# Kernel tuning notes

Hardware: AMD Instinct MI355X
Metric: run time of the kernel (lower is better)

The kernel has to match this reference:

```python
import jax, jax.numpy as jnp
import numpy as np

B, N = 1, 1024
VOCAB = 32000
DIM = 512
DEPTH = 2
HEADS = 8
DIM_HEAD = 64
DIM_INNER = HEADS * DIM_HEAD      # 512
DIM_FF = 4 * DIM                  # 2048
MAX_SEQ = 1024
EPS = 1e-12


def sq_dist(x, w):
    # squared L2 distance between rows of x [..., d] and rows of w [m, d] -> [..., m]
    xs = jnp.sum(x * x, axis=-1, keepdims=True)
    ws = jnp.sum(w * w, axis=-1)
    return xs - 2.0 * jnp.einsum('...d,md->...m', x, w) + ws


def cdist(x, w):
    # euclidean distance (torch.cdist equivalent)
    return jnp.sqrt(jnp.maximum(sq_dist(x, w), 0.0))


def rmsnorm(x, gamma):
    # F.normalize(x, dim=-1) * sqrt(dim) * (gamma + 1)
    n = jnp.linalg.norm(x, axis=-1, keepdims=True)
    return x / jnp.maximum(n, EPS) * (DIM ** 0.5) * (gamma + 1.0)


def attention(x, qkv_w, out_w):
    b, n, _ = x.shape
    qkv = cdist(x, qkv_w)                                   # [b, n, 3*inner] (to_qkv: squared=False)
    qkv = qkv.reshape(b, n, 3, HEADS, DIM_HEAD)
    qkv = qkv.transpose(2, 0, 3, 1, 4)                      # [3, b, h, n, d]
    q, k, v = qkv[0], qkv[1], qkv[2]
    qs = jnp.sum(q * q, axis=-1)                            # [b, h, n]
    ks = jnp.sum(k * k, axis=-1)                            # [b, h, n]
    # -||q_i - k_j||^2 = 2 q.k - ||q||^2 - ||k||^2
    sim = (2.0 * jnp.einsum('bhid,bhjd->bhij', q, k)
           - qs[..., :, None] - ks[..., None, :]) * (DIM_HEAD ** -0.5)
    attn = jax.nn.softmax(sim, axis=-1)
    o = jnp.einsum('bhij,bhjd->bhid', attn, v)
    o = o.transpose(0, 2, 1, 3).reshape(b, n, DIM_INNER)    # merge heads
    return o @ out_w.T                                      # plain Linear, no bias


def feedforward(x, w_in, b_in, w_out):
    h = -sq_dist(x, w_in) + b_in                            # proj_in: squared=True, negate=True, bias
    h = jax.nn.gelu(h, approximate=False)
    return h @ w_out.T                                      # plain Linear, no bias


def setup_inputs() -> dict:
    key = jax.random.key(0)
    ks = jax.random.split(key, 12)
    nrm = lambda k, s: jax.random.normal(k, s, dtype=jnp.float32)
    return {
        'tokens': jax.random.randint(ks[0], (B, N), 0, VOCAB),
        'token_emb': nrm(ks[1], (VOCAB, DIM)),
        'pos_emb': nrm(ks[2], (MAX_SEQ, DIM)),
        'qkv_w': nrm(ks[3], (DEPTH, 3 * DIM_INNER, DIM)),
        'attn_out_w': nrm(ks[4], (DEPTH, DIM, DIM_INNER)) * 0.02,
        'ff_in_w': nrm(ks[5], (DEPTH, DIM_FF, DIM)),
        'ff_in_b': nrm(ks[6], (DEPTH, DIM_FF)),
        'ff_out_w': nrm(ks[7], (DEPTH, DIM, DIM_FF)) * 0.02,
        'attn_gamma': jnp.zeros((DEPTH, DIM), jnp.float32),
        'ff_gamma': jnp.zeros((DEPTH, DIM), jnp.float32),
        'final_gamma': jnp.zeros((DIM,), jnp.float32),
    }


def reference(tokens, token_emb, pos_emb, qkv_w, attn_out_w, ff_in_w, ff_in_b,
              ff_out_w, attn_gamma, ff_gamma, final_gamma):
    n = tokens.shape[-1]
    x = token_emb[tokens] + pos_emb[:n]                     # [b, n, dim]
    for l in range(DEPTH):
        x = attention(rmsnorm(x, attn_gamma[l]), qkv_w[l], attn_out_w[l]) + x
        x = feedforward(rmsnorm(x, ff_gamma[l]), ff_in_w[l], ff_in_b[l], ff_out_w[l]) + x
    x = rmsnorm(x, final_gamma)
    return -sq_dist(x, token_emb)                           # [b, n, vocab] logits
```

## Files before the change

### kernel.cpp

```cpp
#include <hip/hip_runtime.h>
#include <math.h>

#define DIMM  512
#define NSEQ  1024
#define NHEAD 8
#define DH    64
#define DFF   2048
#define NVOC  32000
#define NDEPTH 2
#define VCENTER 32.0f
#define KVB   64
#define QBLK  32
#define QKOFF ((size_t)NHEAD * NSEQ * DH)
#define FLASH_BLOCKS (NSEQ / QBLK * NHEAD)
#define CONV_ROWS_PER_LAYER (NVOC / NDEPTH)
#define CONV_BLOCKS (CONV_ROWS_PER_LAYER / 64)

typedef __attribute__((ext_vector_type(8))) __bf16 bf16x8;
typedef __attribute__((ext_vector_type(4))) __bf16 bf16x4;
typedef __attribute__((ext_vector_type(4))) float f32x4;

__device__ __forceinline__ void g2l16(const void* g, void* l) {
    __builtin_amdgcn_global_load_lds(
        (const __attribute__((address_space(1))) void*)g,
        (__attribute__((address_space(3))) void*)l, 16, 0, 0);
}

#define WAITV(N) asm volatile("s_waitcnt vmcnt(" #N ")" ::: "memory")

__launch_bounds__(256)
__global__ void embed_rms(const int* __restrict__ tokens,
                          const float* __restrict__ temb,
                          const float* __restrict__ pemb,
                          const float* __restrict__ gamma,
                          float* __restrict__ x,
                          __bf16* __restrict__ y, float* __restrict__ xs) {
    int i = blockIdx.x;
    int tid = threadIdx.x;
    int tok = tokens[i];
    const float* e = temb + (size_t)tok * DIMM;
    const float* p = pemb + (size_t)i * DIMM;
    float v0 = e[tid] + p[tid];
    float v1 = e[tid + 256] + p[tid + 256];
    x[(size_t)i * DIMM + tid]       = v0;
    x[(size_t)i * DIMM + tid + 256] = v1;
    float ss = v0 * v0 + v1 * v1;
    __shared__ float red[4];
    #pragma unroll
    for (int off = 32; off; off >>= 1) ss += __shfl_down(ss, off, 64);
    if ((tid & 63) == 0) red[tid >> 6] = ss;
    __syncthreads();
    float tot = red[0] + red[1] + red[2] + red[3];
    float scale = 22.627416997969522f / fmaxf(sqrtf(tot), 1e-12f);
    float y0 = v0 * scale * (gamma[tid] + 1.0f);
    float y1 = v1 * scale * (gamma[tid + 256] + 1.0f);
    y[(size_t)i * DIMM + tid]       = (__bf16)y0;
    y[(size_t)i * DIMM + tid + 256] = (__bf16)y1;
    float s2 = y0 * y0 + y1 * y1;
    __syncthreads();
    #pragma unroll
    for (int off = 32; off; off >>= 1) s2 += __shfl_down(s2, off, 64);
    if ((tid & 63) == 0) red[tid >> 6] = s2;
    __syncthreads();
    if (tid == 0) xs[i] = red[0] + red[1] + red[2] + red[3];
}

template<int S>
__launch_bounds__(256)
__global__ void rms_red(const float* __restrict__ parts, float* __restrict__ x,
                        const float* __restrict__ gamma,
                        __bf16* __restrict__ y, float* __restrict__ xs) {
    int i = blockIdx.x;
    int tid = threadIdx.x;
    float* xr = x + (size_t)i * DIMM;
    float v0 = xr[tid], v1 = xr[tid + 256];
    #pragma unroll
    for (int s = 0; s < S; s++) {
        const float* pr = parts + (size_t)s * NSEQ * DIMM + (size_t)i * DIMM;
        v0 += pr[tid];
        v1 += pr[tid + 256];
    }
    xr[tid] = v0;
    xr[tid + 256] = v1;
    float ss = v0 * v0 + v1 * v1;
    __shared__ float red[4];
    #pragma unroll
    for (int off = 32; off; off >>= 1) ss += __shfl_down(ss, off, 64);
    if ((tid & 63) == 0) red[tid >> 6] = ss;
    __syncthreads();
    float tot = red[0] + red[1] + red[2] + red[3];
    float scale = 22.627416997969522f / fmaxf(sqrtf(tot), 1e-12f);
    float y0 = v0 * scale * (gamma[tid] + 1.0f);
    float y1 = v1 * scale * (gamma[tid + 256] + 1.0f);
    y[(size_t)i * DIMM + tid]       = (__bf16)y0;
    y[(size_t)i * DIMM + tid + 256] = (__bf16)y1;
    float s2 = y0 * y0 + y1 * y1;
    __syncthreads();
    #pragma unroll
    for (int off = 32; off; off >>= 1) s2 += __shfl_down(s2, off, 64);
    if ((tid & 63) == 0) red[tid >> 6] = s2;
    __syncthreads();
    if (tid == 0) xs[i] = red[0] + red[1] + red[2] + red[3];
}

__launch_bounds__(256)
__global__ void conv_all(const float* __restrict__ qkv_w, const float* __restrict__ attn_out_w,
                         const float* __restrict__ ff_in_w, const float* __restrict__ ff_out_w,
                         __bf16* __restrict__ wq16, __bf16* __restrict__ wa16,
                         __bf16* __restrict__ wfi16, __bf16* __restrict__ wfo16,
                         float* __restrict__ wsq_qkv, float* __restrict__ wsq_ff) {
    int bid = blockIdx.x;
    const float* src; __bf16* dst; float* ssq; int K = DIMM;
    if (bid < NDEPTH * 3 * DIMM) {
        src = qkv_w;  dst = wq16;  ssq = wsq_qkv;
    } else if ((bid -= NDEPTH * 3 * DIMM) < NDEPTH * DIMM) {
        src = attn_out_w; dst = wa16; ssq = nullptr;
    } else if ((bid -= NDEPTH * DIMM) < NDEPTH * DFF) {
        src = ff_in_w; dst = wfi16; ssq = wsq_ff;
    } else {
        bid -= NDEPTH * DFF;
        src = ff_out_w; dst = wfo16; ssq = nullptr; K = DFF;
    }
    const float* s = src + (size_t)bid * K;
    __bf16* d = dst + (size_t)bid * K;
    float ss = 0.f;
    for (int j = threadIdx.x; j < K; j += 256) {
        float v = s[j];
        d[j] = (__bf16)v;
        ss += v * v;
    }
    __shared__ float red[4];
    #pragma unroll
    for (int off = 32; off; off >>= 1) ss += __shfl_down(ss, off, 64);
    if ((threadIdx.x & 63) == 0) red[threadIdx.x >> 6] = ss;
    __syncthreads();
    if (threadIdx.x == 0 && ssq) ssq[bid] = red[0] + red[1] + red[2] + red[3];
}

enum { MODE_LINEAR = 0, MODE_CDIST = 1, MODE_FFGELU = 2, MODE_LOGITS = 3 };

template<int MODE>
__device__ __forceinline__ void write_elem(void* Cout, int r, int c, int M, float dot,
                                           float xsr, const float* __restrict__ ws,
                                           const float* __restrict__ bias) {
    if (MODE == MODE_LINEAR) {
        ((float*)Cout)[(size_t)r * M + c] = dot;
    } else if (MODE == MODE_FFGELU) {
        float d2 = xsr + ws[c] - 2.0f * dot;
        float hh = -d2 + bias[c];
        float v = 0.5f * hh * (1.0f + erff(hh * 0.70710678118654752f));
        ((__bf16*)Cout)[(size_t)r * M + c] = (__bf16)v;
    }
}

__launch_bounds__(512)
__global__ void gemm_logits(const __bf16* __restrict__ A, const __bf16* __restrict__ W,
                            const float* __restrict__ xs, const float* __restrict__ ws,
                            float* __restrict__ out) {
    __shared__ __align__(16) __bf16 As[6 * 128 * 32];
    __shared__ __align__(16) __bf16 Bs[6 * 256 * 32];
    const int tid = threadIdx.x;
    const int lane = tid & 63;
    const int wv = tid >> 6;
    const int wr = wv >> 2, wc = wv & 3;

    int id = blockIdx.x;
    id = (id & 7) * 125 + (id >> 3);
    const int row0 = (id & 7) * 128;
    const int col0 = (id >> 3) * 256;

    const int scol = ((tid & 3) ^ ((tid >> 3) & 3)) * 8;
    const __bf16* gA = A + (size_t)(row0 + (tid >> 2)) * DIMM + scol;
    const __bf16* gB = W + (size_t)(col0 + (tid >> 2)) * DIMM + scol;
    const int lrow = lane & 15;
    const int l4 = lane >> 4;
    const int slot = (l4 ^ ((lrow >> 1) & 3)) * 8;

    auto stageChunk = [&](int k0, int b) {
        g2l16(gA + k0,                      &As[b * 4096 + tid * 8]);
        g2l16(gB + k0,                      &Bs[b * 8192 + tid * 8]);
        g2l16(gB + (size_t)128 * DIMM + k0, &Bs[b * 8192 + 4096 + tid * 8]);
    };

    f32x4 acc[4][4] = {};
    const int nP = DIMM >> 6;
    stageChunk(0, 0);  stageChunk(32, 1);
    stageChunk(64, 2); stageChunk(96, 3);
    int pb = 0;
    for (int p = 0; p < nP; p++) {
        if (p < nP - 1) WAITV(6); else WAITV(0);
        __builtin_amdgcn_s_barrier();
        __builtin_amdgcn_sched_barrier(0);
        if (p + 2 < nP) {
            int nb = pb + 2; if (nb >= 3) nb -= 3;
            stageChunk((p + 2) << 6,        nb * 2);
            stageChunk(((p + 2) << 6) + 32, nb * 2 + 1);
        }
        #pragma unroll
        for (int half = 0; half < 2; half++) {
            const int b = pb * 2 + half;
            bf16x8 af[4], bfr[4];
            #pragma unroll
            for (int m = 0; m < 4; m++)
                af[m] = *(const bf16x8*)&As[b * 4096 + (wr * 64 + m * 16 + lrow) * 32 + slot];
            #pragma unroll
            for (int n = 0; n < 4; n++)
                bfr[n] = *(const bf16x8*)&Bs[b * 8192 + (wc * 64 + n * 16 + lrow) * 32 + slot];
            #pragma unroll
            for (int m = 0; m < 4; m++)
                #pragma unroll
                for (int n = 0; n < 4; n++)
                    acc[m][n] = __builtin_amdgcn_mfma_f32_16x16x32_bf16(af[m], bfr[n], acc[m][n], 0, 0, 0);
        }
        if (++pb == 3) pb = 0;
    }

    const int r_base = row0 + wr * 64 + l4 * 4;
    const int c_base = col0 + wc * 64 + lrow;
    #pragma unroll
    for (int m = 0; m < 4; m++)
        #pragma unroll
        for (int j = 0; j < 4; j++) {
            const int r = r_base + m * 16 + j;
            const float xsr = xs[r];
            #pragma unroll
            for (int n = 0; n < 4; n++) {
                const int c = c_base + n * 16;
                out[(size_t)r * NVOC + c] = -(xsr + ws[c] - 2.0f * acc[m][n][j]);
            }
        }
}

template<int MODE>
__launch_bounds__(256)
__global__ void gemm64(const __bf16* __restrict__ A, const __bf16* __restrict__ W,
                       const float* __restrict__ xs, const float* __restrict__ ws,
                       const float* __restrict__ bias,
                       void* __restrict__ Cout, int K, int Kstr, int M,
                       float* __restrict__ ksout) {
    __shared__ __align__(16) __bf16 As[6 * 64 * 32];
    __shared__ __align__(16) __bf16 Bs[6 * 64 * 32];
    __shared__ float ksred[2][64];
    const int tid = threadIdx.x;
    const int lane = tid & 63;
    const int wv = tid >> 6;
    const int wr = wv >> 1, wc = wv & 1;

    const int gx = gridDim.x;
    const int total = gx * gridDim.y;
    int id = blockIdx.y * gx + blockIdx.x;
    id = (id & 7) * (total >> 3) + (id >> 3);
    const int bx = id % gx;
    const int by = id / gx;
    const int row0 = by * 64;
    const int col0 = bx * 64;
    const size_t zoff = (size_t)blockIdx.z * K;
    float* Cz = (float*)Cout + (size_t)blockIdx.z * NSEQ * M;

    const int scol = (((tid & 3) ^ ((tid >> 3) & 3))) * 8;
    const __bf16* gA = A + (size_t)(row0 + (tid >> 2)) * Kstr + scol + zoff;
    const __bf16* gB = W + (size_t)(col0 + (tid >> 2)) * Kstr + scol + zoff;
    const int lrow = lane & 15;
    const int l4 = lane >> 4;
    const int slot = (l4 ^ ((lrow >> 1) & 3)) * 8;

    auto stageChunk = [&](int k0, int b) {
        g2l16(gA + k0, &As[b * 2048 + tid * 8]);
        g2l16(gB + k0, &Bs[b * 2048 + tid * 8]);
    };

    f32x4 acc[2][2] = {};
    const int nP = K >> 6;
    stageChunk(0, 0);  stageChunk(32, 1);
    stageChunk(64, 2); stageChunk(96, 3);
    int pb = 0;
    for (int p = 0; p < nP; p++) {
        if (p < nP - 1) WAITV(4); else WAITV(0);
        __builtin_amdgcn_s_barrier();
        __builtin_amdgcn_sched_barrier(0);
        if (p + 2 < nP) {
            int nb = pb + 2; if (nb >= 3) nb -= 3;
            stageChunk((p + 2) << 6,        nb * 2);
            stageChunk(((p + 2) << 6) + 32, nb * 2 + 1);
        }
        #pragma unroll
        for (int half = 0; half < 2; half++) {
            const int b = pb * 2 + half;
            bf16x8 af[2], bfr[2];
            #pragma unroll
            for (int m = 0; m < 2; m++)
                af[m] = *(const bf16x8*)&As[b * 2048 + (wr * 32 + m * 16 + lrow) * 32 + slot];
            #pragma unroll
            for (int n = 0; n < 2; n++)
                bfr[n] = *(const bf16x8*)&Bs[b * 2048 + (wc * 32 + n * 16 + lrow) * 32 + slot];
            #pragma unroll
            for (int m = 0; m < 2; m++)
                #pragma unroll
                for (int n = 0; n < 2; n++)
                    acc[m][n] = __builtin_amdgcn_mfma_f32_16x16x32_bf16(af[m], bfr[n], acc[m][n], 0, 0, 0);
        }
        if (++pb == 3) pb = 0;
    }

    const int r_base = row0 + wr * 32 + (lane >> 4) * 4;
    const int c_base = col0 + wc * 32 + (lane & 15);

    if (MODE == MODE_CDIST) {
        const int sec = col0 >> 9;
        const int h = (col0 >> 6) & 7;
        __bf16* Qc = (__bf16*)Cout;
        float pk[2][4];
        #pragma unroll
        for (int m = 0; m < 2; m++)
            #pragma unroll
            for (int j = 0; j < 4; j++) {
                const int r = r_base + m * 16 + j;
                const float xsr = xs[r];
                pk[m][j] = 0.f;
                #pragma unroll
                for (int n = 0; n < 2; n++) {
                    const int c = c_base + n * 16;
                    float d2 = xsr + ws[c] - 2.0f * acc[m][n][j];
                    float v = sqrtf(fmaxf(d2, 0.0f)) - VCENTER;
                    __bf16 bv = (__bf16)v;
                    const int d = c & 63;
                    if (sec == 0)      Qc[((size_t)h * NSEQ + r) * DH + d] = bv;
                    else if (sec == 1) Qc[QKOFF + ((size_t)h * NSEQ + r) * DH + d] = bv;
                    else               Qc[2 * QKOFF + ((size_t)h * DH + d) * NSEQ + r] = bv;
                    float fv = (float)bv;
                    pk[m][j] += fv * fv;
                }
            }
        if (sec == 1) {
            #pragma unroll
            for (int m = 0; m < 2; m++)
                #pragma unroll
                for (int j = 0; j < 4; j++) {
                    float v = pk[m][j];
                    #pragma unroll
                    for (int off = 1; off < 16; off <<= 1) v += __shfl_xor(v, off, 64);
                    if (lrow == 0) ksred[wc][wr * 32 + m * 16 + l4 * 4 + j] = v;
                }
            __syncthreads();
            if (tid < 64)
                ksout[(size_t)h * NSEQ + row0 + tid] = ksred[0][tid] + ksred[1][tid];
        }
    } else {
        #pragma unroll
        for (int m = 0; m < 2; m++)
            #pragma unroll
            for (int j = 0; j < 4; j++) {
                const int r = r_base + m * 16 + j;
                const float xsr = (MODE == MODE_LINEAR) ? 0.f : xs[r];
                #pragma unroll
                for (int n = 0; n < 2; n++)
                    write_elem<MODE>(Cz, r, c_base + n * 16, M, acc[m][n][j], xsr, ws, bias);
            }
    }
}

__launch_bounds__(128)
__global__ void flash_attn(const __bf16* __restrict__ Qc, const __bf16* __restrict__ Kc,
                           const __bf16* __restrict__ VcT, const float* __restrict__ ks,
                           __bf16* __restrict__ O,
                           const float* __restrict__ temb, __bf16* __restrict__ temb16,
                           float* __restrict__ wsq_temb, int conv_row0) {
    const int tid = threadIdx.x, lane = tid & 63, wv = tid >> 6;

    if (blockIdx.x >= FLASH_BLOCKS) {
        const int base = conv_row0 + (blockIdx.x - FLASH_BLOCKS) * 64;
        for (int it = 0; it < 32; it++) {
            const int row = base + it * 2 + wv;
            const float* src = temb + (size_t)row * DIMM;
            float4 a = ((const float4*)src)[lane];
            float4 b2 = ((const float4*)src)[lane + 64];
            float ss = a.x * a.x + a.y * a.y + a.z * a.z + a.w * a.w
                     + b2.x * b2.x + b2.y * b2.y + b2.z * b2.z + b2.w * b2.w;
            bf16x4 oa, ob;
            oa.x = (__bf16)a.x;  oa.y = (__bf16)a.y;  oa.z = (__bf16)a.z;  oa.w = (__bf16)a.w;
            ob.x = (__bf16)b2.x; ob.y = (__bf16)b2.y; ob.z = (__bf16)b2.z; ob.w = (__bf16)b2.w;
            *(bf16x4*)&temb16[(size_t)row * DIMM + lane * 4]       = oa;
            *(bf16x4*)&temb16[(size_t)row * DIMM + 256 + lane * 4] = ob;
            #pragma unroll
            for (int off = 32; off; off >>= 1) ss += __shfl_down(ss, off, 64);
            if (lane == 0) wsq_temb[row] = ss;
        }
        return;
    }

    __shared__ __align__(16) __bf16 Qs[QBLK * 64];
    __shared__ __align__(16) __bf16 Ks[2][64 * 64];
    __shared__ __align__(16) __bf16 Vs[2][64 * 64];
    __shared__ __align__(16) __bf16 Ps[2][16 * 64];
    __shared__ float kss[2][64];
    const int h = blockIdx.x >> 5, q0 = (blockIdx.x & 31) * QBLK;
    const int l15 = lane & 15, l4 = lane >> 4;

    #pragma unroll
    for (int pass = 0; pass < 2; pass++) {
        int gl = tid + pass * 128, r = gl >> 3, gs = (gl & 7) ^ (r & 7);
        g2l16(Qc + ((size_t)h * NSEQ + q0 + r) * DH + gs * 8, &Qs[gl * 8]);
    }
    auto stage = [&](int c, int buf) {
        const int kv0 = c * KVB;
        #pragma unroll
        for (int pass = 0; pass < 4; pass++) {
            int gl = tid + pass * 128, r = gl >> 3, gs = (gl & 7) ^ (r & 7);
            g2l16(Kc + ((size_t)h * NSEQ + kv0 + r) * DH + gs * 8, &Ks[buf][gl * 8]);
            g2l16(VcT + ((size_t)h * DH + r) * NSEQ + kv0 + gs * 8, &Vs[buf][gl * 8]);
        }
        if (tid < KVB) kss[buf][tid] = ks[(size_t)h * NSEQ + c * KVB + tid];
    };
    stage(0, 0);
    __syncthreads();

    bf16x8 qf[2];
    #pragma unroll
    for (int s = 0; s < 2; s++) {
        int row = wv * 16 + l15;
        int g = (l4 + 4 * s) ^ (row & 7);
        qf[s] = *(const bf16x8*)&Qs[row * 64 + g * 8];
    }

    float m_j[4], l_j[4];
    f32x4 o_[4] = {};
    #pragma unroll
    for (int j = 0; j < 4; j++) { m_j[j] = -1e30f; l_j[j] = 0.f; }

    for (int c = 0; c < NSEQ / KVB; c++) {
        const int b = c & 1;
        if (c + 1 < NSEQ / KVB) stage(c + 1, b ^ 1);

        f32x4 sa[4] = {};
        #pragma unroll
        for (int s = 0; s < 2; s++) {
            bf16x8 kf[4];
            #pragma unroll
            for (int n = 0; n < 4; n++) {
                int row = n * 16 + l15;
                int g = (l4 + 4 * s) ^ (row & 7);
                kf[n] = *(const bf16x8*)&Ks[b][row * 64 + g * 8];
            }
            #pragma unroll
            for (int n = 0; n < 4; n++)
                sa[n] = __builtin_amdgcn_mfma_f32_16x16x32_bf16(qf[s], kf[n], sa[n], 0, 0, 0);
        }
        float ksv[4];
        #pragma unroll
        for (int n = 0; n < 4; n++) ksv[n] = kss[b][n * 16 + l15];

        float scale[4];
        #pragma unroll
        for (int j = 0; j < 4; j++) {
            float mx = -1e30f;
            #pragma unroll
            for (int n = 0; n < 4; n++) {
                float sv = sa[n][j] * 0.25f - ksv[n] * 0.125f;
                sa[n][j] = sv;
                mx = fmaxf(mx, sv);
            }
            #pragma unroll
            for (int off = 1; off < 16; off <<= 1) mx = fmaxf(mx, __shfl_xor(mx, off, 64));
            float mn = fmaxf(m_j[j], mx);
            scale[j] = expf(m_j[j] - mn);
            m_j[j] = mn;
        }
        #pragma unroll
        for (int j = 0; j < 4; j++) {
            const int row = l4 * 4 + j;
            float ls = 0.f;
            #pragma unroll
            for (int n = 0; n < 4; n++) {
                float pv = expf(sa[n][j] - m_j[j]);
                ls += pv;
                int col = n * 16 + l15;
                Ps[wv][row * 64 + ((((col >> 3) ^ (row & 7)) << 3) | (col & 7))] = (__bf16)pv;
            }
            #pragma unroll
            for (int off = 1; off < 16; off <<= 1) ls += __shfl_xor(ls, off, 64);
            l_j[j] = l_j[j] * scale[j] + ls;
            o_[0][j] *= scale[j]; o_[1][j] *= scale[j];
            o_[2][j] *= scale[j]; o_[3][j] *= scale[j];
        }

        #pragma unroll
        for (int s = 0; s < 2; s++) {
            int g = (l4 + 4 * s) ^ (l15 & 7);
            bf16x8 pf = *(const bf16x8*)&Ps[wv][l15 * 64 + g * 8];
            #pragma unroll
            for (int n = 0; n < 4; n++) {
                int row = n * 16 + l15;
                int gv = (l4 + 4 * s) ^ (row & 7);
                bf16x8 vf = *(const bf16x8*)&Vs[b][row * 64 + gv * 8];
                o_[n] = __builtin_amdgcn_mfma_f32_16x16x32_bf16(pf, vf, o_[n], 0, 0, 0);
            }
        }
        __syncthreads();
    }

    #pragma unroll
    for (int n = 0; n < 4; n++)
        #pragma unroll
        for (int j = 0; j < 4; j++) {
            int row = q0 + wv * 16 + l4 * 4 + j;
            int d = n * 16 + l15;
            O[(size_t)row * DIMM + h * DH + d] = (__bf16)(o_[n][j] / l_j[j] + VCENTER);
        }
}

extern "C" void kernel_launch(void* const* d_in, const int* in_sizes, int n_in,
                              void* d_out, int out_size, void* d_ws, size_t ws_size,
                              hipStream_t stream) {
    (void)in_sizes; (void)n_in; (void)out_size; (void)ws_size;
    const int*   tokens      = (const int*)d_in[0];
    const float* temb        = (const float*)d_in[1];
    const float* pemb        = (const float*)d_in[2];
    const float* qkv_w       = (const float*)d_in[3];
    const float* attn_out_w  = (const float*)d_in[4];
    const float* ff_in_w     = (const float*)d_in[5];
    const float* ff_in_b     = (const float*)d_in[6];
    const float* ff_out_w    = (const float*)d_in[7];
    const float* attn_gamma  = (const float*)d_in[8];
    const float* ff_gamma    = (const float*)d_in[9];
    const float* final_gamma = (const float*)d_in[10];
    float* out = (float*)d_out;

    char* p = (char*)d_ws;
    float*  x        = (float*)p;  p += (size_t)NSEQ * DIMM * 4;
    float*  xs       = (float*)p;  p += (size_t)NSEQ * 4;
    float*  wsq_qkv  = (float*)p;  p += (size_t)NDEPTH * 3 * DIMM * 4;
    float*  wsq_ff   = (float*)p;  p += (size_t)NDEPTH * DFF * 4;
    float*  wsq_temb = (float*)p;  p += (size_t)NVOC * 4;
    float*  ksbuf    = (float*)p;  p += (size_t)NHEAD * NSEQ * 4;
    float*  parts    = (float*)p;  p += (size_t)4 * NSEQ * DIMM * 4;
    __bf16* y16      = (__bf16*)p; p += (size_t)NSEQ * DIMM * 2;
    __bf16* o16      = (__bf16*)p; p += (size_t)NSEQ * DIMM * 2;
    __bf16* Qc       = (__bf16*)p; p += 3 * QKOFF * 2;
    __bf16* hb16     = (__bf16*)p; p += (size_t)NSEQ * DFF * 2;
    __bf16* wq16     = (__bf16*)p; p += (size_t)NDEPTH * 3 * DIMM * DIMM * 2;
    __bf16* wa16     = (__bf16*)p; p += (size_t)NDEPTH * DIMM * DIMM * 2;
    __bf16* wfi16    = (__bf16*)p; p += (size_t)NDEPTH * DFF * DIMM * 2;
    __bf16* wfo16    = (__bf16*)p; p += (size_t)NDEPTH * DIMM * DFF * 2;
    __bf16* temb16   = (__bf16*)p; p += (size_t)NVOC * DIMM * 2;
    __bf16* Kc  = Qc + QKOFF;
    __bf16* VcT = Qc + 2 * QKOFF;

    const int convBlocks = NDEPTH * 3 * DIMM + NDEPTH * DIMM + NDEPTH * DFF
                         + NDEPTH * DIMM;
    conv_all<<<convBlocks, 256, 0, stream>>>(qkv_w, attn_out_w, ff_in_w, ff_out_w,
                                             wq16, wa16, wfi16, wfo16,
                                             wsq_qkv, wsq_ff);

    embed_rms<<<NSEQ, 256, 0, stream>>>(tokens, temb, pemb, attn_gamma, x, y16, xs);

    for (int l = 0; l < NDEPTH; l++) {
        const __bf16* qkvw = wq16  + (size_t)l * 3 * DIMM * DIMM;
        const __bf16* aow  = wa16  + (size_t)l * DIMM * DIMM;
        const __bf16* fiw  = wfi16 + (size_t)l * DFF * DIMM;
        const __bf16* fow  = wfo16 + (size_t)l * DIMM * DFF;
        const float*  fib  = ff_in_b + (size_t)l * DFF;
        const float*  next_gamma = (l + 1 < NDEPTH) ? (attn_gamma + (l + 1) * DIMM)
                                                    : final_gamma;

        gemm64<MODE_CDIST><<<dim3(3 * DIMM / 64, NSEQ / 64), 256, 0, stream>>>(
            y16, qkvw, xs, wsq_qkv + l * 3 * DIMM, nullptr, Qc, DIMM, DIMM, 3 * DIMM, ksbuf);
        flash_attn<<<FLASH_BLOCKS + CONV_BLOCKS, 128, 0, stream>>>(
            Qc, Kc, VcT, ksbuf, o16, temb, temb16, wsq_temb, l * CONV_ROWS_PER_LAYER);
        gemm64<MODE_LINEAR><<<dim3(DIMM / 64, NSEQ / 64, 2), 256, 0, stream>>>(
            o16, aow, nullptr, nullptr, nullptr, parts, DIMM / 2, DIMM, DIMM, nullptr);
        rms_red<2><<<NSEQ, 256, 0, stream>>>(parts, x, ff_gamma + l * DIMM, y16, xs);

        gemm64<MODE_FFGELU><<<dim3(DFF / 64, NSEQ / 64), 256, 0, stream>>>(
            y16, fiw, xs, wsq_ff + l * DFF, fib, hb16, DIMM, DIMM, DFF, nullptr);
        gemm64<MODE_LINEAR><<<dim3(DIMM / 64, NSEQ / 64, 4), 256, 0, stream>>>(
            hb16, fow, nullptr, nullptr, nullptr, parts, DFF / 4, DFF, DIMM, nullptr);
        rms_red<4><<<NSEQ, 256, 0, stream>>>(parts, x, next_gamma, y16, xs);
    }

    gemm_logits<<<1000, 512, 0, stream>>>(y16, temb16, xs, wsq_temb, out);
}
```

Before: 232.2 us.

## Stage logits epilogue through LDS for coalesced stores; merge conv and embed kernels

```diff
diff --git a/kernel.cpp b/kernel.cpp
--- a/kernel.cpp
+++ b/kernel.cpp
@@ -15,6 +15,7 @@
 #define FLASH_BLOCKS (NSEQ / QBLK * NHEAD)
 #define CONV_ROWS_PER_LAYER (NVOC / NDEPTH)
 #define CONV_BLOCKS (CONV_ROWS_PER_LAYER / 64)
+#define CONVW_BLOCKS (NDEPTH * 3 * DIMM + NDEPTH * DIMM + NDEPTH * DFF + NDEPTH * DIMM)
 
 typedef __attribute__((ext_vector_type(8))) __bf16 bf16x8;
 typedef __attribute__((ext_vector_type(4))) __bf16 bf16x4;
@@ -29,86 +30,48 @@
 #define WAITV(N) asm volatile("s_waitcnt vmcnt(" #N ")" ::: "memory")
 
 __launch_bounds__(256)
-__global__ void embed_rms(const int* __restrict__ tokens,
-                          const float* __restrict__ temb,
-                          const float* __restrict__ pemb,
-                          const float* __restrict__ gamma,
-                          float* __restrict__ x,
-                          __bf16* __restrict__ y, float* __restrict__ xs) {
-    int i = blockIdx.x;
-    int tid = threadIdx.x;
-    int tok = tokens[i];
-    const float* e = temb + (size_t)tok * DIMM;
-    const float* p = pemb + (size_t)i * DIMM;
-    float v0 = e[tid] + p[tid];
-    float v1 = e[tid + 256] + p[tid + 256];
-    x[(size_t)i * DIMM + tid]       = v0;
-    x[(size_t)i * DIMM + tid + 256] = v1;
-    float ss = v0 * v0 + v1 * v1;
+__global__ void conv_embed(const float* __restrict__ qkv_w, const float* __restrict__ attn_out_w,
+                           const float* __restrict__ ff_in_w, const float* __restrict__ ff_out_w,
+                           __bf16* __restrict__ wq16, __bf16* __restrict__ wa16,
+                           __bf16* __restrict__ wfi16, __bf16* __restrict__ wfo16,
+                           float* __restrict__ wsq_qkv, float* __restrict__ wsq_ff,
+                           const int* __restrict__ tokens, const float* __restrict__ temb,
+                           const float* __restrict__ pemb, const float* __restrict__ gamma,
+                           float* __restrict__ x, __bf16* __restrict__ y,
+                           float* __restrict__ xs) {
+    const int tid = threadIdx.x;
     __shared__ float red[4];
-    #pragma unroll
-    for (int off = 32; off; off >>= 1) ss += __shfl_down(ss, off, 64);
-    if ((tid & 63) == 0) red[tid >> 6] = ss;
-    __syncthreads();
-    float tot = red[0] + red[1] + red[2] + red[3];
-    float scale = 22.627416997969522f / fmaxf(sqrtf(tot), 1e-12f);
-    float y0 = v0 * scale * (gamma[tid] + 1.0f);
-    float y1 = v1 * scale * (gamma[tid + 256] + 1.0f);
-    y[(size_t)i * DIMM + tid]       = (__bf16)y0;
-    y[(size_t)i * DIMM + tid + 256] = (__bf16)y1;
-    float s2 = y0 * y0 + y1 * y1;
-    __syncthreads();
-    #pragma unroll
-    for (int off = 32; off; off >>= 1) s2 += __shfl_down(s2, off, 64);
-    if ((tid & 63) == 0) red[tid >> 6] = s2;
-    __syncthreads();
-    if (tid == 0) xs[i] = red[0] + red[1] + red[2] + red[3];
-}
-
-template<int S>
-__launch_bounds__(256)
-__global__ void rms_red(const float* __restrict__ parts, float* __restrict__ x,
-                        const float* __restrict__ gamma,
-                        __bf16* __restrict__ y, float* __restrict__ xs) {
-    int i = blockIdx.x;
-    int tid = threadIdx.x;
-    float* xr = x + (size_t)i * DIMM;
-    float v0 = xr[tid], v1 = xr[tid + 256];
-    #pragma unroll
-    for (int s = 0; s < S; s++) {
-        const float* pr = parts + (size_t)s * NSEQ * DIMM + (size_t)i * DIMM;
-        v0 += pr[tid];
-        v1 += pr[tid + 256];
-    }
-    xr[tid] = v0;
-    xr[tid + 256] = v1;
-    float ss = v0 * v0 + v1 * v1;
-    __shared__ float red[4];
-    #pragma unroll
-    for (int off = 32; off; off >>= 1) ss += __shfl_down(ss, off, 64);
-    if ((tid & 63) == 0) red[tid >> 6] = ss;
-    __syncthreads();
-    float tot = red[0] + red[1] + red[2] + red[3];
-    float scale = 22.627416997969522f / fmaxf(sqrtf(tot), 1e-12f);
-    float y0 = v0 * scale * (gamma[tid] + 1.0f);
-    float y1 = v1 * scale * (gamma[tid + 256] + 1.0f);
-    y[(size_t)i * DIMM + tid]       = (__bf16)y0;
-    y[(size_t)i * DIMM + tid + 256] = (__bf16)y1;
-    float s2 = y0 * y0 + y1 * y1;
-    __syncthreads();
-    #pragma unroll
-    for (int off = 32; off; off >>= 1) s2 += __shfl_down(s2, off, 64);
-    if ((tid & 63) == 0) red[tid >> 6] = s2;
-    __syncthreads();
-    if (tid == 0) xs[i] = red[0] + red[1] + red[2] + red[3];
-}
-
-__launch_bounds__(256)
-__global__ void conv_all(const float* __restrict__ qkv_w, const float* __restrict__ attn_out_w,
-                         const float* __restrict__ ff_in_w, const float* __restrict__ ff_out_w,
-                         __bf16* __restrict__ wq16, __bf16* __restrict__ wa16,
-                         __bf16* __restrict__ wfi16, __bf16* __restrict__ wfo16,
-                         float* __restrict__ wsq_qkv, float* __restrict__ wsq_ff) {
+
+    if (blockIdx.x >= CONVW_BLOCKS) {
+        const int i = blockIdx.x - CONVW_BLOCKS;
+        int tok = tokens[i];
+        const float* e = temb + (size_t)tok * DIMM;
+        const float* pp = pemb + (size_t)i * DIMM;
+        float v0 = e[tid] + pp[tid];
+        float v1 = e[tid + 256] + pp[tid + 256];
+        x[(size_t)i * DIMM + tid]       = v0;
+        x[(size_t)i * DIMM + tid + 256] = v1;
+        float ss = v0 * v0 + v1 * v1;
+        #pragma unroll
+        for (int off = 32; off; off >>= 1) ss += __shfl_down(ss, off, 64);
+        if ((tid & 63) == 0) red[tid >> 6] = ss;
+        __syncthreads();
+        float tot = red[0] + red[1] + red[2] + red[3];
+        float scale = 22.627416997969522f / fmaxf(sqrtf(tot), 1e-12f);
+        float y0 = v0 * scale * (gamma[tid] + 1.0f);
+        float y1 = v1 * scale * (gamma[tid + 256] + 1.0f);
+        y[(size_t)i * DIMM + tid]       = (__bf16)y0;
+        y[(size_t)i * DIMM + tid + 256] = (__bf16)y1;
+        float s2 = y0 * y0 + y1 * y1;
+        __syncthreads();
+        #pragma unroll
+        for (int off = 32; off; off >>= 1) s2 += __shfl_down(s2, off, 64);
+        if ((tid & 63) == 0) red[tid >> 6] = s2;
+        __syncthreads();
+        if (tid == 0) xs[i] = red[0] + red[1] + red[2] + red[3];
+        return;
+    }
+
     int bid = blockIdx.x;
     const float* src; __bf16* dst; float* ssq; int K = DIMM;
     if (bid < NDEPTH * 3 * DIMM) {
@@ -124,17 +87,54 @@
     const float* s = src + (size_t)bid * K;
     __bf16* d = dst + (size_t)bid * K;
     float ss = 0.f;
-    for (int j = threadIdx.x; j < K; j += 256) {
+    for (int j = tid; j < K; j += 256) {
         float v = s[j];
         d[j] = (__bf16)v;
         ss += v * v;
     }
+    #pragma unroll
+    for (int off = 32; off; off >>= 1) ss += __shfl_down(ss, off, 64);
+    if ((tid & 63) == 0) red[tid >> 6] = ss;
+    __syncthreads();
+    if (tid == 0 && ssq) ssq[bid] = red[0] + red[1] + red[2] + red[3];
+}
+
+template<int S>
+__launch_bounds__(256)
+__global__ void rms_red(const float* __restrict__ parts, float* __restrict__ x,
+                        const float* __restrict__ gamma,
+                        __bf16* __restrict__ y, float* __restrict__ xs) {
+    int i = blockIdx.x;
+    int tid = threadIdx.x;
+    float* xr = x + (size_t)i * DIMM;
+    float v0 = xr[tid], v1 = xr[tid + 256];
+    #pragma unroll
+    for (int s = 0; s < S; s++) {
+        const float* pr = parts + (size_t)s * NSEQ * DIMM + (size_t)i * DIMM;
+        v0 += pr[tid];
+        v1 += pr[tid + 256];
+    }
+    xr[tid] = v0;
+    xr[tid + 256] = v1;
+    float ss = v0 * v0 + v1 * v1;
     __shared__ float red[4];
     #pragma unroll
     for (int off = 32; off; off >>= 1) ss += __shfl_down(ss, off, 64);
-    if ((threadIdx.x & 63) == 0) red[threadIdx.x >> 6] = ss;
-    __syncthreads();
-    if (threadIdx.x == 0 && ssq) ssq[bid] = red[0] + red[1] + red[2] + red[3];
+    if ((tid & 63) == 0) red[tid >> 6] = ss;
+    __syncthreads();
+    float tot = red[0] + red[1] + red[2] + red[3];
+    float scale = 22.627416997969522f / fmaxf(sqrtf(tot), 1e-12f);
+    float y0 = v0 * scale * (gamma[tid] + 1.0f);
+    float y1 = v1 * scale * (gamma[tid + 256] + 1.0f);
+    y[(size_t)i * DIMM + tid]       = (__bf16)y0;
+    y[(size_t)i * DIMM + tid + 256] = (__bf16)y1;
+    float s2 = y0 * y0 + y1 * y1;
+    __syncthreads();
+    #pragma unroll
+    for (int off = 32; off; off >>= 1) s2 += __shfl_down(s2, off, 64);
+    if ((tid & 63) == 0) red[tid >> 6] = s2;
+    __syncthreads();
+    if (tid == 0) xs[i] = red[0] + red[1] + red[2] + red[3];
 }
 
 enum { MODE_LINEAR = 0, MODE_CDIST = 1, MODE_FFGELU = 2, MODE_LOGITS = 3 };
@@ -157,8 +157,10 @@
 __global__ void gemm_logits(const __bf16* __restrict__ A, const __bf16* __restrict__ W,
                             const float* __restrict__ xs, const float* __restrict__ ws,
                             float* __restrict__ out) {
-    __shared__ __align__(16) __bf16 As[6 * 128 * 32];
-    __shared__ __align__(16) __bf16 Bs[6 * 256 * 32];
+    __shared__ __align__(16) char smem[49152 + 98304];
+    __bf16* As = (__bf16*)smem;
+    __bf16* Bs = (__bf16*)(smem + 49152);
+    float* tile = (float*)smem;
     const int tid = threadIdx.x;
     const int lane = tid & 63;
     const int wv = tid >> 6;
@@ -177,9 +179,9 @@
     const int slot = (l4 ^ ((lrow >> 1) & 3)) * 8;
 
     auto stageChunk = [&](int k0, int b) {
-        g2l16(gA + k0,                      &As[b * 4096 + tid * 8]);
-        g2l16(gB + k0,                      &Bs[b * 8192 + tid * 8]);
-        g2l16(gB + (size_t)128 * DIMM + k0, &Bs[b * 8192 + 4096 + tid * 8]);
+        g2l16(gA + k0,                      As + b * 4096 + tid * 8);
+        g2l16(gB + k0,                      Bs + b * 8192 + tid * 8);
+        g2l16(gB + (size_t)128 * DIMM + k0, Bs + b * 8192 + 4096 + tid * 8);
     };
 
     f32x4 acc[4][4] = {};
@@ -202,10 +204,10 @@
             bf16x8 af[4], bfr[4];
             #pragma unroll
             for (int m = 0; m < 4; m++)
-                af[m] = *(const bf16x8*)&As[b * 4096 + (wr * 64 + m * 16 + lrow) * 32 + slot];
+                af[m] = *(const bf16x8*)(As + b * 4096 + (wr * 64 + m * 16 + lrow) * 32 + slot);
             #pragma unroll
             for (int n = 0; n < 4; n++)
-                bfr[n] = *(const bf16x8*)&Bs[b * 8192 + (wc * 64 + n * 16 + lrow) * 32 + slot];
+                bfr[n] = *(const bf16x8*)(Bs + b * 8192 + (wc * 64 + n * 16 + lrow) * 32 + slot);
             #pragma unroll
             for (int m = 0; m < 4; m++)
                 #pragma unroll
@@ -214,21 +216,31 @@
         }
         if (++pb == 3) pb = 0;
     }
-
-    const int r_base = row0 + wr * 64 + l4 * 4;
-    const int c_base = col0 + wc * 64 + lrow;
+    __syncthreads();
+
     #pragma unroll
     for (int m = 0; m < 4; m++)
         #pragma unroll
         for (int j = 0; j < 4; j++) {
-            const int r = r_base + m * 16 + j;
-            const float xsr = xs[r];
+            const int rl = wr * 64 + m * 16 + l4 * 4 + j;
+            const float xsr = xs[row0 + rl];
+            const int sw = ((rl >> 2) & 3) << 2;
             #pragma unroll
             for (int n = 0; n < 4; n++) {
-                const int c = c_base + n * 16;
-                out[(size_t)r * NVOC + c] = -(xsr + ws[c] - 2.0f * acc[m][n][j]);
-            }
-        }
+                const int cl = wc * 64 + n * 16 + lrow;
+                tile[rl * 256 + (cl ^ sw)] = -(xsr + ws[col0 + cl] - 2.0f * acc[m][n][j]);
+            }
+        }
+    __syncthreads();
+
+    #pragma unroll
+    for (int jj = 0; jj < 16; jj++) {
+        const int f = jj * 2048 + tid * 4;
+        const int rr = f >> 8, cc = f & 255;
+        const int sw = ((rr >> 2) & 3) << 2;
+        f32x4 v = *(const f32x4*)&tile[rr * 256 + (cc ^ sw)];
+        *(f32x4*)&out[(size_t)(row0 + rr) * NVOC + col0 + cc] = v;
+    }
 }
 
 template<int MODE>
@@ -545,13 +557,10 @@
     __bf16* Kc  = Qc + QKOFF;
     __bf16* VcT = Qc + 2 * QKOFF;
 
-    const int convBlocks = NDEPTH * 3 * DIMM + NDEPTH * DIMM + NDEPTH * DFF
-                         + NDEPTH * DIMM;
-    conv_all<<<convBlocks, 256, 0, stream>>>(qkv_w, attn_out_w, ff_in_w, ff_out_w,
-                                             wq16, wa16, wfi16, wfo16,
-                                             wsq_qkv, wsq_ff);
-
-    embed_rms<<<NSEQ, 256, 0, stream>>>(tokens, temb, pemb, attn_gamma, x, y16, xs);
+    conv_embed<<<CONVW_BLOCKS + NSEQ, 256, 0, stream>>>(
+        qkv_w, attn_out_w, ff_in_w, ff_out_w,
+        wq16, wa16, wfi16, wfo16, wsq_qkv, wsq_ff,
+        tokens, temb, pemb, attn_gamma, x, y16, xs);
 
     for (int l = 0; l < NDEPTH; l++) {
         const __bf16* qkvw = wq16  + (size_t)l * 3 * DIMM * DIMM;
```

After: 228.3 us. Within noise of the previous version (-1.7%).
